# Kernel optimization log

Hardware: AMD Instinct MI355X
Metric: run time of the kernel (lower is better)

## Reference

```python
import jax, jax.numpy as jnp
import numpy as np

EMBED_DIM = 1024
NUM_HEADS = 16
HEAD_DIM = EMBED_DIM // NUM_HEADS
MLP_HIDDEN = 4096


def layer_norm(x, gamma, beta, eps=1e-5):
    mu = jnp.mean(x, axis=-1, keepdims=True)
    var = jnp.var(x, axis=-1, keepdims=True)
    return (x - mu) / jnp.sqrt(var + eps) * gamma + beta


def setup_inputs() -> dict:
    key = jax.random.key(0)
    ks = jax.random.split(key, 16)
    d, h = EMBED_DIM, MLP_HIDDEN
    s = 0.02
    inp = {
        "x": jax.random.normal(ks[0], (2, 2048, d), dtype=jnp.float32),
        "ln1_g": jnp.ones((d,), jnp.float32),
        "ln1_b": jnp.zeros((d,), jnp.float32),
        "ln2_g": jnp.ones((d,), jnp.float32),
        "ln2_b": jnp.zeros((d,), jnp.float32),
        "Wq": jax.random.normal(ks[1], (d, d), jnp.float32) * s,
        "bq": jnp.zeros((d,), jnp.float32),
        "Wk": jax.random.normal(ks[2], (d, d), jnp.float32) * s,
        "bk": jnp.zeros((d,), jnp.float32),
        "Wv": jax.random.normal(ks[3], (d, d), jnp.float32) * s,
        "bv": jnp.zeros((d,), jnp.float32),
        "Wo": jax.random.normal(ks[4], (d, d), jnp.float32) * s,
        "bo": jnp.zeros((d,), jnp.float32),
        "W1": jax.random.normal(ks[5], (d, h), jnp.float32) * s,
        "b1": jnp.zeros((h,), jnp.float32),
        "W2": jax.random.normal(ks[6], (h, d), jnp.float32) * s,
        "b2": jnp.zeros((d,), jnp.float32),
    }
    return inp


def reference(x, ln1_g, ln1_b, ln2_g, ln2_b, Wq, bq, Wk, bk, Wv, bv, Wo, bo, W1, b1, W2, b2):
    B, T, C = x.shape
    H, Dh = NUM_HEADS, HEAD_DIM
    # attention branch
    xn = layer_norm(x, ln1_g, ln1_b)
    q = (xn @ Wq + bq).reshape(B, T, H, Dh).transpose(0, 2, 1, 3)  # [B,H,T,Dh]
    k = (xn @ Wk + bk).reshape(B, T, H, Dh).transpose(0, 2, 1, 3)
    v = (xn @ Wv + bv).reshape(B, T, H, Dh).transpose(0, 2, 1, 3)
    scores = jnp.einsum('bhtd,bhsd->bhts', q, k) / jnp.sqrt(jnp.float32(Dh))
    attn = jax.nn.softmax(scores, axis=-1)
    out = jnp.einsum('bhts,bhsd->bhtd', attn, v)
    out = out.transpose(0, 2, 1, 3).reshape(B, T, C)
    x = x + out @ Wo + bo
    # MLP branch
    xn2 = layer_norm(x, ln2_g, ln2_b)
    x = x + jax.nn.relu(xn2 @ W1 + b1) @ W2 + b2
    return x
```

## Files before the change

kernel.cpp:

```cpp
#include <hip/hip_runtime.h>

typedef float f32x4 __attribute__((ext_vector_type(4)));
typedef __bf16 bf16x8 __attribute__((ext_vector_type(8)));

constexpr int TT   = 2048;
constexpr int CC   = 1024;
constexpr int HIDN = 4096;
constexpr int MM   = 4096;
constexpr int NQKV = 3072;

union U84 { uint32_t u[4]; bf16x8 v; };

__device__ inline uint32_t cvt_pk_bf16(float lo, float hi) {
  uint32_t r;
  asm("v_cvt_pk_bf16_f32 %0, %1, %2" : "=v"(r) : "v"(lo), "v"(hi));
  return r;
}
__device__ inline ushort f2bf(float f) { return (ushort)(cvt_pk_bf16(f, 0.f) & 0xffffu); }
__device__ inline float bfbits2f(uint32_t bits) {
  union { uint32_t u; float f; } c; c.u = bits; return c.f;
}
__device__ inline float exp2_fast(float x) {
  float r;
  asm("v_exp_f32 %0, %1" : "=v"(r) : "v"(x));
  return r;
}

#define AS1C(p) ((__attribute__((address_space(1))) void*)(p))
#define AS3(p)  ((__attribute__((address_space(3))) void*)(p))

__global__ __launch_bounds__(256) void prep_weights(const float* __restrict__ Wq,
                                                    const float* __restrict__ Wk,
                                                    const float* __restrict__ Wv,
                                                    const float* __restrict__ Wo,
                                                    const float* __restrict__ W1,
                                                    const float* __restrict__ W2,
                                                    const float* __restrict__ bq,
                                                    const float* __restrict__ bk,
                                                    const float* __restrict__ bv,
                                                    const float* __restrict__ x,
                                                    const float* __restrict__ g1,
                                                    const float* __restrict__ b1v,
                                                    ushort* __restrict__ WqkvT,
                                                    ushort* __restrict__ WoT,
                                                    ushort* __restrict__ W1T,
                                                    ushort* __restrict__ W2T,
                                                    float* __restrict__ Bqkv,
                                                    ushort* __restrict__ Xn) {
  const int id = blockIdx.x;
  const int t = threadIdx.x;
  if (id >= 12300) {
    const int row = id - 12300;
    float4 v = reinterpret_cast<const float4*>(x + (size_t)row * CC)[t];
    float s  = v.x + v.y + v.z + v.w;
    float ss = v.x * v.x + v.y * v.y + v.z * v.z + v.w * v.w;
#pragma unroll
    for (int off = 32; off; off >>= 1) {
      s  += __shfl_down(s, off);
      ss += __shfl_down(ss, off);
    }
    __shared__ float red[16];
    const int wid = t >> 6, lane = t & 63;
    if (lane == 0) { red[wid] = s; red[8 + wid] = ss; }
    __syncthreads();
    if (t == 0) {
      red[0] = red[0] + red[1] + red[2] + red[3];
      red[8] = red[8] + red[9] + red[10] + red[11];
    }
    __syncthreads();
    const float mu   = red[0] * (1.0f / CC);
    const float var  = red[8] * (1.0f / CC) - mu * mu;
    const float rstd = rsqrtf(var + 1e-5f);
    float4 gg = reinterpret_cast<const float4*>(g1)[t];
    float4 bb = reinterpret_cast<const float4*>(b1v)[t];
    uint2 st;
    st.x = cvt_pk_bf16((v.x - mu) * rstd * gg.x + bb.x, (v.y - mu) * rstd * gg.y + bb.y);
    st.y = cvt_pk_bf16((v.z - mu) * rstd * gg.z + bb.z, (v.w - mu) * rstd * gg.w + bb.w);
    *reinterpret_cast<uint2*>(Xn + (size_t)row * CC + t * 4) = st;
    return;
  }
  if (id >= 12288) {
    const int i = (id - 12288) * 256 + t;
    Bqkv[i] = (i < 1024) ? bq[i] : ((i < 2048) ? bk[i - 1024] : bv[i - 2048]);
    return;
  }
  const float* W; ushort* out; int Kd, Nd, bx, by, rowOff = 0;
  if (id < 4096) {
    const int which = id >> 10, sub = id & 1023;
    bx = sub & 31; by = sub >> 5; Kd = 1024; Nd = 1024;
    if (which == 0)      { W = Wq; out = WqkvT; rowOff = 0; }
    else if (which == 1) { W = Wk; out = WqkvT; rowOff = 1024; }
    else if (which == 2) { W = Wv; out = WqkvT; rowOff = 2048; }
    else                 { W = Wo; out = WoT; }
  } else if (id < 8192) {
    const int sub = id - 4096; bx = sub & 127; by = sub >> 7;
    W = W1; out = W1T; Kd = 1024; Nd = 4096;
  } else {
    const int sub = id - 8192; bx = sub & 31; by = sub >> 5;
    W = W2; out = W2T; Kd = 4096; Nd = 1024;
  }
  const int n0 = bx * 32, k0 = by * 32;
  __shared__ float Ts[32][33];
  {
    const int r = t >> 3, cb = (t & 7) * 4;
    float4 v = *reinterpret_cast<const float4*>(W + (size_t)(k0 + r) * Nd + n0 + cb);
    Ts[r][cb + 0] = v.x; Ts[r][cb + 1] = v.y; Ts[r][cb + 2] = v.z; Ts[r][cb + 3] = v.w;
  }
  __syncthreads();
  {
    const int nl = t >> 3, kb = (t & 7) * 4;
    uint2 st;
    st.x = cvt_pk_bf16(Ts[kb + 0][nl], Ts[kb + 1][nl]);
    st.y = cvt_pk_bf16(Ts[kb + 2][nl], Ts[kb + 3][nl]);
    *reinterpret_cast<uint2*>(out + (size_t)(rowOff + n0 + nl) * Kd + k0 + kb) = st;
  }
}

template <int BN, bool RELU, bool VOUT, bool PARTIAL>
__global__ __launch_bounds__(512, 2) void gemm_8w(const ushort* __restrict__ A,
                                                  const ushort* __restrict__ Bt,
                                                  const float* __restrict__ bias,
                                                  ushort* __restrict__ outp,
                                                  ushort* __restrict__ Vt,
                                                  ushort* __restrict__ P1,
                                                  int N, int K, int Kchunk) {
  constexpr int WCOLS = BN / 4;
  constexpr int NF    = WCOLS / 16;
  constexpr int BCH   = BN / 64;
  constexpr int BUFB  = 32768 + BN * 128;
  __shared__ char lds[2 * BUFB];
  const int t = threadIdx.x, lane = t & 63, w = t >> 6;
  const int g = lane >> 4, i16 = lane & 15;
  const int wr = w >> 2, wc = w & 3;
  const int nwg  = gridDim.x * gridDim.y;
  const int orig = blockIdx.y * gridDim.x + blockIdx.x;
  const int sw   = (orig & 7) * (nwg >> 3) + (orig >> 3);
  const int row0 = (sw / gridDim.x) * 256, col0 = (sw % gridDim.x) * BN;
  const int kstart = PARTIAL ? blockIdx.z * Kchunk : 0;
  const int NT = (PARTIAL ? Kchunk : K) >> 6;
  ushort* __restrict__ Out = (PARTIAL && blockIdx.z) ? P1 : outp;

  const ushort* aG[4];
  const ushort* bG[BCH];
#pragma unroll
  for (int i = 0; i < 4; ++i) {
    const int c = t + 512 * i;
    const int r = c >> 3, ssw = (c & 7) ^ (r & 7);
    aG[i] = A + (size_t)(row0 + r) * K + kstart + ssw * 8;
  }
#pragma unroll
  for (int i = 0; i < BCH; ++i) {
    const int c = t + 512 * i;
    const int r = c >> 3, ssw = (c & 7) ^ (r & 7);
    bG[i] = Bt + (size_t)(col0 + r) * K + kstart + ssw * 8;
  }

  int aoff[8][2], boff[NF][2];
#pragma unroll
  for (int mf = 0; mf < 8; ++mf) {
    const int R = wr * 128 + mf * 16 + i16;
#pragma unroll
    for (int kk = 0; kk < 2; ++kk)
      aoff[mf][kk] = R * 128 + (((kk << 2) | g) ^ (R & 7)) * 16;
  }
#pragma unroll
  for (int nf = 0; nf < NF; ++nf) {
    const int Cn = wc * WCOLS + nf * 16 + i16;
#pragma unroll
    for (int kk = 0; kk < 2; ++kk)
      boff[nf][kk] = Cn * 128 + (((kk << 2) | g) ^ (Cn & 7)) * 16;
  }

  f32x4 acc[8][NF] = {};

  auto STAGE = [&](int bi, int kt) {
    char* aB = lds + bi * BUFB;
    char* bB = aB + 32768;
    const int ko = kt * 64;
#pragma unroll
    for (int i = 0; i < 4; ++i)
      __builtin_amdgcn_global_load_lds(AS1C(aG[i] + ko), AS3(aB + i * 8192 + w * 1024), 16, 0, 0);
#pragma unroll
    for (int i = 0; i < BCH; ++i)
      __builtin_amdgcn_global_load_lds(AS1C(bG[i] + ko), AS3(bB + i * 8192 + w * 1024), 16, 0, 0);
  };

  STAGE(0, 0);

  for (int kt = 0; kt < NT; ++kt) {
    const int cur = kt & 1;
    if (kt + 1 < NT) {
      STAGE(cur ^ 1, kt + 1);
      if constexpr (BN == 256)      asm volatile("s_waitcnt vmcnt(8)" ::: "memory");
      else if constexpr (BN == 192) asm volatile("s_waitcnt vmcnt(7)" ::: "memory");
      else                          asm volatile("s_waitcnt vmcnt(6)" ::: "memory");
    } else {
      asm volatile("s_waitcnt vmcnt(0)" ::: "memory");
    }
    asm volatile("s_barrier" ::: "memory");
    __builtin_amdgcn_sched_barrier(0);

    const char* aB = (const char*)lds + cur * BUFB;
    const char* bB = aB + 32768;
    bf16x8 b4[NF][2], a4[4][2];
#pragma unroll
    for (int nf = 0; nf < NF; ++nf)
#pragma unroll
      for (int kk = 0; kk < 2; ++kk)
        b4[nf][kk] = *reinterpret_cast<const bf16x8*>(bB + boff[nf][kk]);
#pragma unroll
    for (int mf = 0; mf < 4; ++mf)
#pragma unroll
      for (int kk = 0; kk < 2; ++kk)
        a4[mf][kk] = *reinterpret_cast<const bf16x8*>(aB + aoff[mf][kk]);
    __builtin_amdgcn_s_setprio(1);
#pragma unroll
    for (int mf = 0; mf < 4; ++mf)
#pragma unroll
      for (int nf = 0; nf < NF; ++nf)
#pragma unroll
        for (int kk = 0; kk < 2; ++kk)
          acc[mf][nf] = __builtin_amdgcn_mfma_f32_16x16x32_bf16(a4[mf][kk], b4[nf][kk], acc[mf][nf], 0, 0, 0);
    __builtin_amdgcn_s_setprio(0);
    asm volatile("s_barrier" ::: "memory");
    __builtin_amdgcn_sched_barrier(0);
#pragma unroll
    for (int mf = 0; mf < 4; ++mf)
#pragma unroll
      for (int kk = 0; kk < 2; ++kk)
        a4[mf][kk] = *reinterpret_cast<const bf16x8*>(aB + aoff[mf + 4][kk]);
    __builtin_amdgcn_s_setprio(1);
#pragma unroll
    for (int mf = 0; mf < 4; ++mf)
#pragma unroll
      for (int nf = 0; nf < NF; ++nf)
#pragma unroll
        for (int kk = 0; kk < 2; ++kk)
          acc[mf + 4][nf] = __builtin_amdgcn_mfma_f32_16x16x32_bf16(a4[mf][kk], b4[nf][kk], acc[mf + 4][nf], 0, 0, 0);
    __builtin_amdgcn_s_setprio(0);
    asm volatile("s_barrier" ::: "memory");
    __builtin_amdgcn_sched_barrier(0);
  }

  const int qcol0 = col0 + wc * WCOLS;

  if constexpr (VOUT) {
#pragma unroll
    for (int nf = 0; nf < NF; ++nf) {
      const int ncol = qcol0 + nf * 16 + i16;
      const float bb = bias[ncol];
      if (ncol >= 2048) {
        const int d = ncol - 2048;
        const int hh = d >> 6, dd = d & 63;
#pragma unroll
        for (int mf = 0; mf < 8; ++mf) {
          const int mrow = row0 + wr * 128 + mf * 16 + 4 * g;
          const int bb_ = mrow >> 11, tok = mrow & 2047;
          uint2 st;
          st.x = cvt_pk_bf16(acc[mf][nf][0] + bb, acc[mf][nf][1] + bb);
          st.y = cvt_pk_bf16(acc[mf][nf][2] + bb, acc[mf][nf][3] + bb);
          *reinterpret_cast<uint2*>(Vt + (size_t)((bb_ * 16 + hh) * 64 + dd) * TT + tok) = st;
        }
      } else {
#pragma unroll
        for (int mf = 0; mf < 8; ++mf) {
          const int mrow = row0 + wr * 128 + mf * 16 + 4 * g;
#pragma unroll
          for (int r = 0; r < 4; ++r)
            Out[(size_t)(mrow + r) * N + ncol] = f2bf(acc[mf][nf][r] + bb);
        }
      }
    }
    return;
  } else if constexpr (BN == 128) {
#pragma unroll
    for (int nf = 0; nf < NF; ++nf) {
      const int ncol = qcol0 + nf * 16 + i16;
#pragma unroll
      for (int mf = 0; mf < 8; ++mf) {
        const int mrow = row0 + wr * 128 + mf * 16 + 4 * g;
#pragma unroll
        for (int r = 0; r < 4; ++r)
          Out[(size_t)(mrow + r) * N + ncol] = f2bf(acc[mf][nf][r]);
      }
    }
    return;
  } else {
    float* Lf = (float*)(lds + w * 4096);
    const int rr2 = lane >> 2, q = lane & 3;
#pragma unroll
    for (int mf = 0; mf < 8; ++mf) {
#pragma unroll
      for (int nf = 0; nf < NF; ++nf)
#pragma unroll
        for (int r = 0; r < 4; ++r) {
          const int row = 4 * g + r;
          Lf[row * 64 + ((16 * nf + i16) ^ ((row & 7) << 2))] = acc[mf][nf][r];
        }
      asm volatile("s_waitcnt lgkmcnt(0)" ::: "memory");
      uint32_t u[8];
#pragma unroll
      for (int j = 0; j < 4; ++j) {
        f32x4 v = *reinterpret_cast<const f32x4*>(Lf + rr2 * 64 + ((q * 16 + 4 * j) ^ ((rr2 & 7) << 2)));
        float e0 = v[0], e1 = v[1], e2 = v[2], e3 = v[3];
        if (!PARTIAL) {
          const float4 b4v = *reinterpret_cast<const float4*>(bias + qcol0 + q * 16 + 4 * j);
          e0 += b4v.x; e1 += b4v.y; e2 += b4v.z; e3 += b4v.w;
          if (RELU) {
            e0 = fmaxf(e0, 0.f); e1 = fmaxf(e1, 0.f);
            e2 = fmaxf(e2, 0.f); e3 = fmaxf(e3, 0.f);
          }
        }
        u[2 * j + 0] = cvt_pk_bf16(e0, e1);
        u[2 * j + 1] = cvt_pk_bf16(e2, e3);
      }
      const int mrow = row0 + wr * 128 + mf * 16 + rr2;
      ushort* orow = Out + (size_t)mrow * N + qcol0 + q * 16;
      uint4 s0; s0.x = u[0]; s0.y = u[1]; s0.z = u[2]; s0.w = u[3];
      uint4 s1; s1.x = u[4]; s1.y = u[5]; s1.z = u[6]; s1.w = u[7];
      *reinterpret_cast<uint4*>(orow) = s0;
      *reinterpret_cast<uint4*>(orow + 8) = s1;
      asm volatile("s_waitcnt lgkmcnt(0)" ::: "memory");
    }
  }
}

__device__ inline float bfsum2(uint32_t a, uint32_t b, bool hi) {
  if (hi) return bfbits2f(a & 0xffff0000u) + bfbits2f(b & 0xffff0000u);
  return bfbits2f(a << 16) + bfbits2f(b << 16);
}

__global__ __launch_bounds__(256) void reduce_wo_ln(const ushort* __restrict__ P0,
                                                    const ushort* __restrict__ P1,
                                                    const float* __restrict__ x,
                                                    const float* __restrict__ bo,
                                                    const float* __restrict__ g,
                                                    const float* __restrict__ b,
                                                    ushort* __restrict__ X1b,
                                                    ushort* __restrict__ Xn) {
  const int row = blockIdx.x, t = threadIdx.x;
  const size_t off = (size_t)row * CC + t * 4;
  float4 v  = *reinterpret_cast<const float4*>(x + off);
  const uint2 q0 = *reinterpret_cast<const uint2*>(P0 + off);
  const uint2 q1 = *reinterpret_cast<const uint2*>(P1 + off);
  float4 bb = reinterpret_cast<const float4*>(bo)[t];
  v.x += bfsum2(q0.x, q1.x, false) + bb.x;
  v.y += bfsum2(q0.x, q1.x, true)  + bb.y;
  v.z += bfsum2(q0.y, q1.y, false) + bb.z;
  v.w += bfsum2(q0.y, q1.y, true)  + bb.w;
  {
    uint2 st;
    st.x = cvt_pk_bf16(v.x, v.y);
    st.y = cvt_pk_bf16(v.z, v.w);
    *reinterpret_cast<uint2*>(X1b + off) = st;
  }

  float s  = v.x + v.y + v.z + v.w;
  float ss = v.x * v.x + v.y * v.y + v.z * v.z + v.w * v.w;
#pragma unroll
  for (int o = 32; o; o >>= 1) {
    s  += __shfl_down(s, o);
    ss += __shfl_down(ss, o);
  }
  __shared__ float red[16];
  const int wid = t >> 6, lane = t & 63;
  if (lane == 0) { red[wid] = s; red[8 + wid] = ss; }
  __syncthreads();
  if (t == 0) {
    red[0] = red[0] + red[1] + red[2] + red[3];
    red[8] = red[8] + red[9] + red[10] + red[11];
  }
  __syncthreads();
  const float mu   = red[0] * (1.0f / CC);
  const float var  = red[8] * (1.0f / CC) - mu * mu;
  const float rstd = rsqrtf(var + 1e-5f);
  float4 gg = reinterpret_cast<const float4*>(g)[t];
  float4 lb = reinterpret_cast<const float4*>(b)[t];
  uint2 st;
  st.x = cvt_pk_bf16((v.x - mu) * rstd * gg.x + lb.x, (v.y - mu) * rstd * gg.y + lb.y);
  st.y = cvt_pk_bf16((v.z - mu) * rstd * gg.z + lb.z, (v.w - mu) * rstd * gg.w + lb.w);
  *reinterpret_cast<uint2*>(Xn + off) = st;
}

__global__ __launch_bounds__(256) void reduce_fc2(const ushort* __restrict__ P0,
                                                  const ushort* __restrict__ P1,
                                                  const ushort* __restrict__ X1b,
                                                  const float* __restrict__ b2,
                                                  float* __restrict__ out) {
  const int row = blockIdx.x, t = threadIdx.x;
  const size_t off = (size_t)row * CC + t * 4;
  const uint2 x1 = *reinterpret_cast<const uint2*>(X1b + off);
  const uint2 q0 = *reinterpret_cast<const uint2*>(P0 + off);
  const uint2 q1 = *reinterpret_cast<const uint2*>(P1 + off);
  float4 bb = reinterpret_cast<const float4*>(b2)[t];
  float4 v;
  v.x = bfbits2f(x1.x << 16)         + bfsum2(q0.x, q1.x, false) + bb.x;
  v.y = bfbits2f(x1.x & 0xffff0000u) + bfsum2(q0.x, q1.x, true)  + bb.y;
  v.z = bfbits2f(x1.y << 16)         + bfsum2(q0.y, q1.y, false) + bb.z;
  v.w = bfbits2f(x1.y & 0xffff0000u) + bfsum2(q0.y, q1.y, true)  + bb.w;
  *reinterpret_cast<float4*>(out + off) = v;
}

__global__ __launch_bounds__(512, 4) void attn_full(const ushort* __restrict__ qkv,
                                                    const ushort* __restrict__ Vt,
                                                    ushort* __restrict__ attnb) {
  __shared__ ushort Ks[2][4096];
  __shared__ ushort Vs[2][4096];
  __shared__ uint32_t Ps[8][16][36];
  const int t = threadIdx.x, lane = t & 63, w = t >> 6;
  const int g = lane >> 4, iq = lane & 15;
  const int flat = blockIdx.x;
  const int work = (flat & 7) * 64 + (flat >> 3);
  const int bh = work >> 4;
  const int qt = work & 15;
  const int b = bh >> 4, h = bh & 15;

  bf16x8 qfrag[2];
  {
    const ushort* qrow = qkv + (size_t)(b * TT + qt * 128 + w * 16 + iq) * NQKV + h * 64;
    const float qs = 0.125f * 1.44269504f;
#pragma unroll
    for (int kk = 0; kk < 2; ++kk) {
      uint4 raw = *reinterpret_cast<const uint4*>(qrow + kk * 32 + g * 8);
      uint32_t rr[4] = {raw.x, raw.y, raw.z, raw.w};
      U84 tmp;
#pragma unroll
      for (int c = 0; c < 4; ++c) {
        float lo = bfbits2f(rr[c] << 16) * qs;
        float hi = bfbits2f(rr[c] & 0xffff0000u) * qs;
        tmp.u[c] = cvt_pk_bf16(lo, hi);
      }
      qfrag[kk] = tmp.v;
    }
  }

  const int sr1 = t >> 3, sc1 = t & 7;
  const int csw = (sc1 ^ (sr1 & 7)) * 8;
  const ushort* kbase = qkv + 1024 + h * 64;
  const ushort* vbase = Vt + (size_t)(bh * 64) * TT;

  auto STAGE = [&](int bi, int kt) {
    const size_t tok = (size_t)(b * TT + kt * 64);
    __builtin_amdgcn_global_load_lds(AS1C(kbase + (tok + sr1) * NQKV + csw),
                                     AS3((char*)&Ks[bi][0] + w * 1024), 16, 0, 0);
    __builtin_amdgcn_global_load_lds(AS1C(vbase + (size_t)sr1 * TT + kt * 64 + csw),
                                     AS3((char*)&Vs[bi][0] + w * 1024), 16, 0, 0);
  };

  uint32_t (*pw)[36] = Ps[w];
  const int wsw = (iq & 8) << 1;
  const int xsb = wsw << 2;
  const char* prow = (const char*)&pw[iq][0];

  float lrun = 0.f;
  f32x4 ot[4] = {};

  constexpr int NKT = TT / 64;
  STAGE(0, 0);

  for (int kt = 0; kt < NKT; ++kt) {
    const int cur = kt & 1;
    if (kt + 1 < NKT) {
      STAGE(cur ^ 1, kt + 1);
      asm volatile("s_waitcnt vmcnt(2)" ::: "memory");
    } else {
      asm volatile("s_waitcnt vmcnt(0)" ::: "memory");
    }
    asm volatile("s_barrier" ::: "memory");
    __builtin_amdgcn_sched_barrier(0);
    const char* Kc = (const char*)&Ks[cur][0];
    const char* Vc = (const char*)&Vs[cur][0];

    f32x4 sfr[4] = {};
    __builtin_amdgcn_s_setprio(1);
#pragma unroll
    for (int kk = 0; kk < 2; ++kk)
#pragma unroll
      for (int jf = 0; jf < 4; ++jf) {
        const int row = iq + 16 * jf;
        const int off = row * 128 + ((kk * 64 + g * 16) ^ ((row & 7) << 4));
        bf16x8 a = *reinterpret_cast<const bf16x8*>(Kc + off);
        sfr[jf] = __builtin_amdgcn_mfma_f32_16x16x32_bf16(a, qfrag[kk], sfr[jf], 0, 0, 0);
      }
    __builtin_amdgcn_s_setprio(0);

#pragma unroll
    for (int f = 0; f < 4; ++f) {
      float p0 = exp2_fast(sfr[f][0]);
      float p1 = exp2_fast(sfr[f][1]);
      float p2 = exp2_fast(sfr[f][2]);
      float p3 = exp2_fast(sfr[f][3]);
      lrun += (p0 + p1) + (p2 + p3);
      uint2 st2;
      st2.x = cvt_pk_bf16(p0, p1);
      st2.y = cvt_pk_bf16(p2, p3);
      *reinterpret_cast<uint2*>(&pw[iq][(8 * f + 2 * g) ^ wsw]) = st2;
    }
    asm volatile("s_waitcnt lgkmcnt(0)" ::: "memory");

    __builtin_amdgcn_s_setprio(1);
#pragma unroll
    for (int kk = 0; kk < 2; ++kk) {
      bf16x8 pb = *reinterpret_cast<const bf16x8*>(prow + ((kk * 64 + g * 16) ^ xsb));
#pragma unroll
      for (int df = 0; df < 4; ++df) {
        const int row = iq + 16 * df;
        const int off = row * 128 + ((kk * 64 + g * 16) ^ ((row & 7) << 4));
        bf16x8 a = *reinterpret_cast<const bf16x8*>(Vc + off);
        ot[df] = __builtin_amdgcn_mfma_f32_16x16x32_bf16(a, pb, ot[df], 0, 0, 0);
      }
    }
    __builtin_amdgcn_s_setprio(0);

    asm volatile("s_barrier" ::: "memory");
    __builtin_amdgcn_sched_barrier(0);
  }

  lrun += __shfl_xor(lrun, 16, 64);
  lrun += __shfl_xor(lrun, 32, 64);
  const int grow = b * TT + qt * 128 + w * 16 + iq;
  const float inv = 1.f / lrun;
  ushort* orow = attnb + (size_t)grow * CC + h * 64;
#pragma unroll
  for (int df = 0; df < 4; ++df) {
    uint2 st;
    st.x = cvt_pk_bf16(ot[df][0] * inv, ot[df][1] * inv);
    st.y = cvt_pk_bf16(ot[df][2] * inv, ot[df][3] * inv);
    *reinterpret_cast<uint2*>(orow + df * 16 + g * 4) = st;
  }
}

extern "C" void kernel_launch(void* const* d_in, const int* in_sizes, int n_in,
                              void* d_out, int out_size, void* d_ws, size_t ws_size,
                              hipStream_t stream) {
  const float* x     = (const float*)d_in[0];
  const float* ln1_g = (const float*)d_in[1];
  const float* ln1_b = (const float*)d_in[2];
  const float* ln2_g = (const float*)d_in[3];
  const float* ln2_b = (const float*)d_in[4];
  const float* Wq = (const float*)d_in[5];
  const float* bq = (const float*)d_in[6];
  const float* Wk = (const float*)d_in[7];
  const float* bk = (const float*)d_in[8];
  const float* Wv = (const float*)d_in[9];
  const float* bv = (const float*)d_in[10];
  const float* Wo = (const float*)d_in[11];
  const float* bo = (const float*)d_in[12];
  const float* W1 = (const float*)d_in[13];
  const float* b1 = (const float*)d_in[14];
  const float* W2 = (const float*)d_in[15];
  const float* b2 = (const float*)d_in[16];
  float* out = (float*)d_out;
  char* ws = (char*)d_ws;

  ushort* WqkvT = (ushort*)(ws + 0);
  ushort* WoT   = (ushort*)(ws + 6291456);
  ushort* W1T   = (ushort*)(ws + 8388608);
  ushort* W2T   = (ushort*)(ws + 16777216);
  float*  Bqkv  = (float*) (ws + 25165824);
  ushort* Xn    = (ushort*)(ws + 25178112);
  ushort* Attn  = (ushort*)(ws + 33566720);
  ushort* X1b   = (ushort*)(ws + 41955328);
  ushort* Qkv   = (ushort*)(ws + 58732544);
  ushort* Vtb   = (ushort*)(ws + 83898368);
  ushort* Hid   = (ushort*)(ws + 58732544);
  ushort* WoP0  = (ushort*)(ws + 58732544);
  ushort* WoP1  = (ushort*)(ws + 67121152);
  ushort* F2P0  = (ushort*)(ws + 0);
  ushort* F2P1  = (ushort*)(ws + 8388608);

  const dim3 blk(256);

  prep_weights<<<dim3(16396), blk, 0, stream>>>(Wq, Wk, Wv, Wo, W1, W2, bq, bk, bv,
                                                x, ln1_g, ln1_b,
                                                WqkvT, WoT, W1T, W2T, Bqkv, Xn);
  gemm_8w<192, false, true, false><<<dim3(16, 16), dim3(512), 0, stream>>>(
      Xn, WqkvT, Bqkv, Qkv, Vtb, nullptr, NQKV, 1024, 0);
  attn_full<<<dim3(512), dim3(512), 0, stream>>>(Qkv, Vtb, Attn);
  gemm_8w<128, false, false, true><<<dim3(8, 16, 2), dim3(512), 0, stream>>>(
      Attn, WoT, nullptr, WoP0, nullptr, WoP1, 1024, 1024, 512);
  reduce_wo_ln<<<dim3(MM), blk, 0, stream>>>(WoP0, WoP1, x, bo, ln2_g, ln2_b, X1b, Xn);
  gemm_8w<256, true, false, false><<<dim3(16, 16), dim3(512), 0, stream>>>(
      Xn, W1T, b1, Hid, nullptr, nullptr, HIDN, 1024, 0);
  gemm_8w<128, false, false, true><<<dim3(8, 16, 2), dim3(512), 0, stream>>>(
      Hid, W2T, nullptr, F2P0, nullptr, F2P1, 1024, 4096, 2048);
  reduce_fc2<<<dim3(MM), blk, 0, stream>>>(F2P0, F2P1, X1b, b2, out);
}
```

Before: 213.3 us.

## Split attention over key range into three partials with a combine kernel

Attention now runs in two steps. Each block handles 256 query rows instead of 128, reusing each staged K/V tile for two query halves, and covers only a third of the key range. This gives 768 blocks instead of 512 for better occupancy across the CUs. A new combine kernel sums the three unnormalized bf16 partial outputs and their row sums, then normalizes. The cost is an extra launch, the extra partial-buffer traffic, and bf16 rounding of the partials and the row sums.

Measured after the change: 225.2 us. 5.6% more time.

```diff
diff --git a/kernel.cpp b/kernel.cpp
--- a/kernel.cpp
+++ b/kernel.cpp
@@ -20,6 +20,7 @@
 __device__ inline float bfbits2f(uint32_t bits) {
   union { uint32_t u; float f; } c; c.u = bits; return c.f;
 }
+__device__ inline float bf2f(ushort u) { return bfbits2f((uint32_t)u << 16); }
 __device__ inline float exp2_fast(float x) {
   float r;
   asm("v_exp_f32 %0, %1" : "=v"(r) : "v"(x));
@@ -401,23 +402,30 @@
   *reinterpret_cast<float4*>(out + off) = v;
 }
 
-__global__ __launch_bounds__(512, 4) void attn_full(const ushort* __restrict__ qkv,
-                                                    const ushort* __restrict__ Vt,
-                                                    ushort* __restrict__ attnb) {
+__global__ __launch_bounds__(512, 4) void attn_partial(const ushort* __restrict__ qkv,
+                                                       const ushort* __restrict__ Vt,
+                                                       ushort* __restrict__ O0,
+                                                       ushort* __restrict__ O1,
+                                                       ushort* __restrict__ O2,
+                                                       ushort* __restrict__ lbuf) {
   __shared__ ushort Ks[2][4096];
   __shared__ ushort Vs[2][4096];
   __shared__ uint32_t Ps[8][16][36];
   const int t = threadIdx.x, lane = t & 63, w = t >> 6;
   const int g = lane >> 4, iq = lane & 15;
   const int flat = blockIdx.x;
-  const int work = (flat & 7) * 64 + (flat >> 3);
-  const int bh = work >> 4;
-  const int qt = work & 15;
+  const int work = (flat & 7) * 96 + (flat >> 3);
+  const int bh = work / 24;
+  const int rem = work % 24;
+  const int z = rem >> 3;
+  const int qt = rem & 7;
   const int b = bh >> 4, h = bh & 15;
-
-  bf16x8 qfrag[2];
-  {
-    const ushort* qrow = qkv + (size_t)(b * TT + qt * 128 + w * 16 + iq) * NQKV + h * 64;
+  ushort* __restrict__ Obuf = (z == 0) ? O0 : (z == 1) ? O1 : O2;
+
+  bf16x8 qfrag[2][2];
+#pragma unroll
+  for (int qh = 0; qh < 2; ++qh) {
+    const ushort* qrow = qkv + (size_t)(b * TT + qt * 256 + w * 32 + qh * 16 + iq) * NQKV + h * 64;
     const float qs = 0.125f * 1.44269504f;
 #pragma unroll
     for (int kk = 0; kk < 2; ++kk) {
@@ -430,7 +438,7 @@
         float hi = bfbits2f(rr[c] & 0xffff0000u) * qs;
         tmp.u[c] = cvt_pk_bf16(lo, hi);
       }
-      qfrag[kk] = tmp.v;
+      qfrag[qh][kk] = tmp.v;
     }
   }
 
@@ -452,15 +460,16 @@
   const int xsb = wsw << 2;
   const char* prow = (const char*)&pw[iq][0];
 
-  float lrun = 0.f;
-  f32x4 ot[4] = {};
-
-  constexpr int NKT = TT / 64;
-  STAGE(0, 0);
-
-  for (int kt = 0; kt < NKT; ++kt) {
-    const int cur = kt & 1;
-    if (kt + 1 < NKT) {
+  float lrun[2] = {0.f, 0.f};
+  f32x4 ot[2][4] = {};
+
+  const int kt0 = (z == 0) ? 0 : (z == 1) ? 11 : 22;
+  const int ktE = (z == 2) ? 32 : kt0 + 11;
+  STAGE(0, kt0);
+
+  for (int kt = kt0; kt < ktE; ++kt) {
+    const int cur = (kt - kt0) & 1;
+    if (kt + 1 < ktE) {
       STAGE(cur ^ 1, kt + 1);
       asm volatile("s_waitcnt vmcnt(2)" ::: "memory");
     } else {
@@ -471,63 +480,96 @@
     const char* Kc = (const char*)&Ks[cur][0];
     const char* Vc = (const char*)&Vs[cur][0];
 
-    f32x4 sfr[4] = {};
-    __builtin_amdgcn_s_setprio(1);
-#pragma unroll
-    for (int kk = 0; kk < 2; ++kk)
-#pragma unroll
-      for (int jf = 0; jf < 4; ++jf) {
-        const int row = iq + 16 * jf;
-        const int off = row * 128 + ((kk * 64 + g * 16) ^ ((row & 7) << 4));
-        bf16x8 a = *reinterpret_cast<const bf16x8*>(Kc + off);
-        sfr[jf] = __builtin_amdgcn_mfma_f32_16x16x32_bf16(a, qfrag[kk], sfr[jf], 0, 0, 0);
+#pragma unroll
+    for (int qh = 0; qh < 2; ++qh) {
+      f32x4 sfr[4] = {};
+      __builtin_amdgcn_s_setprio(1);
+#pragma unroll
+      for (int kk = 0; kk < 2; ++kk)
+#pragma unroll
+        for (int jf = 0; jf < 4; ++jf) {
+          const int row = iq + 16 * jf;
+          const int off = row * 128 + ((kk * 64 + g * 16) ^ ((row & 7) << 4));
+          bf16x8 a = *reinterpret_cast<const bf16x8*>(Kc + off);
+          sfr[jf] = __builtin_amdgcn_mfma_f32_16x16x32_bf16(a, qfrag[qh][kk], sfr[jf], 0, 0, 0);
+        }
+      __builtin_amdgcn_s_setprio(0);
+
+#pragma unroll
+      for (int f = 0; f < 4; ++f) {
+        float p0 = exp2_fast(sfr[f][0]);
+        float p1 = exp2_fast(sfr[f][1]);
+        float p2 = exp2_fast(sfr[f][2]);
+        float p3 = exp2_fast(sfr[f][3]);
+        lrun[qh] += (p0 + p1) + (p2 + p3);
+        uint2 st2;
+        st2.x = cvt_pk_bf16(p0, p1);
+        st2.y = cvt_pk_bf16(p2, p3);
+        *reinterpret_cast<uint2*>(&pw[iq][(8 * f + 2 * g) ^ wsw]) = st2;
       }
-    __builtin_amdgcn_s_setprio(0);
-
-#pragma unroll
-    for (int f = 0; f < 4; ++f) {
-      float p0 = exp2_fast(sfr[f][0]);
-      float p1 = exp2_fast(sfr[f][1]);
-      float p2 = exp2_fast(sfr[f][2]);
-      float p3 = exp2_fast(sfr[f][3]);
-      lrun += (p0 + p1) + (p2 + p3);
-      uint2 st2;
-      st2.x = cvt_pk_bf16(p0, p1);
-      st2.y = cvt_pk_bf16(p2, p3);
-      *reinterpret_cast<uint2*>(&pw[iq][(8 * f + 2 * g) ^ wsw]) = st2;
-    }
-    asm volatile("s_waitcnt lgkmcnt(0)" ::: "memory");
-
-    __builtin_amdgcn_s_setprio(1);
-#pragma unroll
-    for (int kk = 0; kk < 2; ++kk) {
-      bf16x8 pb = *reinterpret_cast<const bf16x8*>(prow + ((kk * 64 + g * 16) ^ xsb));
-#pragma unroll
-      for (int df = 0; df < 4; ++df) {
-        const int row = iq + 16 * df;
-        const int off = row * 128 + ((kk * 64 + g * 16) ^ ((row & 7) << 4));
-        bf16x8 a = *reinterpret_cast<const bf16x8*>(Vc + off);
-        ot[df] = __builtin_amdgcn_mfma_f32_16x16x32_bf16(a, pb, ot[df], 0, 0, 0);
+      asm volatile("s_waitcnt lgkmcnt(0)" ::: "memory");
+
+      __builtin_amdgcn_s_setprio(1);
+#pragma unroll
+      for (int kk = 0; kk < 2; ++kk) {
+        bf16x8 pb = *reinterpret_cast<const bf16x8*>(prow + ((kk * 64 + g * 16) ^ xsb));
+#pragma unroll
+        for (int df = 0; df < 4; ++df) {
+          const int row = iq + 16 * df;
+          const int off = row * 128 + ((kk * 64 + g * 16) ^ ((row & 7) << 4));
+          bf16x8 a = *reinterpret_cast<const bf16x8*>(Vc + off);
+          ot[qh][df] = __builtin_amdgcn_mfma_f32_16x16x32_bf16(a, pb, ot[qh][df], 0, 0, 0);
+        }
       }
-    }
-    __builtin_amdgcn_s_setprio(0);
+      __builtin_amdgcn_s_setprio(0);
+    }
 
     asm volatile("s_barrier" ::: "memory");
     __builtin_amdgcn_sched_barrier(0);
   }
 
-  lrun += __shfl_xor(lrun, 16, 64);
-  lrun += __shfl_xor(lrun, 32, 64);
-  const int grow = b * TT + qt * 128 + w * 16 + iq;
-  const float inv = 1.f / lrun;
-  ushort* orow = attnb + (size_t)grow * CC + h * 64;
-#pragma unroll
-  for (int df = 0; df < 4; ++df) {
-    uint2 st;
-    st.x = cvt_pk_bf16(ot[df][0] * inv, ot[df][1] * inv);
-    st.y = cvt_pk_bf16(ot[df][2] * inv, ot[df][3] * inv);
-    *reinterpret_cast<uint2*>(orow + df * 16 + g * 4) = st;
-  }
+#pragma unroll
+  for (int qh = 0; qh < 2; ++qh) {
+    float l = lrun[qh];
+    l += __shfl_xor(l, 16, 64);
+    l += __shfl_xor(l, 32, 64);
+    const int grow = b * TT + qt * 256 + w * 32 + qh * 16 + iq;
+    ushort* orow = Obuf + (size_t)grow * CC + h * 64;
+#pragma unroll
+    for (int df = 0; df < 4; ++df) {
+      uint2 st;
+      st.x = cvt_pk_bf16(ot[qh][df][0], ot[qh][df][1]);
+      st.y = cvt_pk_bf16(ot[qh][df][2], ot[qh][df][3]);
+      *reinterpret_cast<uint2*>(orow + df * 16 + g * 4) = st;
+    }
+    if (g == 0)
+      lbuf[((size_t)z * MM + grow) * 16 + h] = f2bf(l);
+  }
+}
+
+__global__ __launch_bounds__(256) void attn_combine(const ushort* __restrict__ O0,
+                                                    const ushort* __restrict__ O1,
+                                                    const ushort* __restrict__ O2,
+                                                    const ushort* __restrict__ lbuf,
+                                                    ushort* __restrict__ attnb) {
+  const int row = blockIdx.x, t = threadIdx.x;
+  const int h = t >> 4;
+  const float l = bf2f(lbuf[(size_t)row * 16 + h]) +
+                  bf2f(lbuf[((size_t)MM + row) * 16 + h]) +
+                  bf2f(lbuf[((size_t)2 * MM + row) * 16 + h]);
+  const float inv = 1.f / l;
+  const size_t off = (size_t)row * CC + t * 4;
+  const uint2 r0 = *reinterpret_cast<const uint2*>(O0 + off);
+  const uint2 r1 = *reinterpret_cast<const uint2*>(O1 + off);
+  const uint2 r2 = *reinterpret_cast<const uint2*>(O2 + off);
+  const float o0 = (bfbits2f(r0.x << 16) + bfbits2f(r1.x << 16) + bfbits2f(r2.x << 16)) * inv;
+  const float o1 = (bfbits2f(r0.x & 0xffff0000u) + bfbits2f(r1.x & 0xffff0000u) + bfbits2f(r2.x & 0xffff0000u)) * inv;
+  const float o2 = (bfbits2f(r0.y << 16) + bfbits2f(r1.y << 16) + bfbits2f(r2.y << 16)) * inv;
+  const float o3 = (bfbits2f(r0.y & 0xffff0000u) + bfbits2f(r1.y & 0xffff0000u) + bfbits2f(r2.y & 0xffff0000u)) * inv;
+  uint2 st;
+  st.x = cvt_pk_bf16(o0, o1);
+  st.y = cvt_pk_bf16(o2, o3);
+  *reinterpret_cast<uint2*>(attnb + off) = st;
 }
 
 extern "C" void kernel_launch(void* const* d_in, const int* in_sizes, int n_in,
@@ -564,6 +606,10 @@
   ushort* Qkv   = (ushort*)(ws + 58732544);
   ushort* Vtb   = (ushort*)(ws + 83898368);
   ushort* Hid   = (ushort*)(ws + 58732544);
+  ushort* OP0   = (ushort*)(ws + 50343936);
+  ushort* OP1   = (ushort*)(ws + 25178112);
+  ushort* OP2   = (ushort*)(ws + 33566720);
+  ushort* lbuf  = (ushort*)(ws + 41955328);
   ushort* WoP0  = (ushort*)(ws + 58732544);
   ushort* WoP1  = (ushort*)(ws + 67121152);
   ushort* F2P0  = (ushort*)(ws + 0);
@@ -576,7 +622,8 @@
                                                 WqkvT, WoT, W1T, W2T, Bqkv, Xn);
   gemm_8w<192, false, true, false><<<dim3(16, 16), dim3(512), 0, stream>>>(
       Xn, WqkvT, Bqkv, Qkv, Vtb, nullptr, NQKV, 1024, 0);
-  attn_full<<<dim3(512), dim3(512), 0, stream>>>(Qkv, Vtb, Attn);
+  attn_partial<<<dim3(768), dim3(512), 0, stream>>>(Qkv, Vtb, OP0, OP1, OP2, lbuf);
+  attn_combine<<<dim3(MM), blk, 0, stream>>>(OP0, OP1, OP2, lbuf, Attn);
   gemm_8w<128, false, false, true><<<dim3(8, 16, 2), dim3(512), 0, stream>>>(
       Attn, WoT, nullptr, WoP0, nullptr, WoP1, 1024, 1024, 512);
   reduce_wo_ln<<<dim3(MM), blk, 0, stream>>>(WoP0, WoP1, x, bo, ln2_g, ln2_b, X1b, Xn);
```
